# Kernel optimization log

Hardware: AMD Instinct MI355X
Metric: run time of the kernel (lower is better)

## Reference

```python
import jax, jax.numpy as jnp
import numpy as np

IOU_THRESHOLD = 0.5


def _make_boxes(key, n, canvas=800.0, min_size=8.0, max_size=160.0):
    k1, k2 = jax.random.split(key)
    cxy = jax.random.uniform(k1, (n, 2), dtype=jnp.float32) * canvas
    wh = min_size + jax.random.uniform(k2, (n, 2), dtype=jnp.float32) * (max_size - min_size)
    return jnp.concatenate([cxy - 0.5 * wh, cxy + 0.5 * wh], axis=1)  # [n,4] x1,y1,x2,y2


def setup_inputs() -> dict:
    key = jax.random.key(0)
    kp, kg, kl = jax.random.split(key, 3)
    N, M = 262144, 256
    proposals = _make_boxes(kp, N)
    gt_boxes = _make_boxes(kg, M)
    gt_labels = jax.random.randint(kl, (M,), 1, 21, dtype=jnp.int64)  # foreground classes 1..20
    return {"proposals": proposals, "gt_boxes": gt_boxes, "gt_labels": gt_labels}


def box_iou(a, b):
    # a: [N,4], b: [M,4] in x1,y1,x2,y2 -> [N,M]
    area_a = (a[:, 2] - a[:, 0]) * (a[:, 3] - a[:, 1])
    area_b = (b[:, 2] - b[:, 0]) * (b[:, 3] - b[:, 1])
    lt = jnp.maximum(a[:, None, :2], b[None, :, :2])
    rb = jnp.minimum(a[:, None, 2:], b[None, :, 2:])
    wh = jnp.clip(rb - lt, 0.0)
    inter = wh[..., 0] * wh[..., 1]
    union = area_a[:, None] + area_b[None, :] - inter
    return inter / union


def encode_boxes(props, gts):
    pw = props[:, 2] - props[:, 0]
    ph = props[:, 3] - props[:, 1]
    px = props[:, 0] + 0.5 * pw
    py = props[:, 1] + 0.5 * ph
    gw = gts[:, 2] - gts[:, 0]
    gh = gts[:, 3] - gts[:, 1]
    gx = gts[:, 0] + 0.5 * gw
    gy = gts[:, 1] + 0.5 * gh
    tx = (gx - px) / pw
    ty = (gy - py) / ph
    tw = jnp.log(gw / pw)
    th = jnp.log(gh / ph)
    return jnp.stack([tx, ty, tw, th], axis=1)


@jax.jit
def reference(proposals, gt_boxes, gt_labels):
    iou = box_iou(proposals, gt_boxes)            # [N,M] -- the memory-bound intermediate
    max_iou = jnp.max(iou, axis=1)                # [N]
    max_idx = jnp.argmax(iou, axis=1)             # [N]
    pos_mask = max_iou >= IOU_THRESHOLD
    roi_labels = jnp.where(pos_mask, gt_labels[max_idx], jnp.zeros_like(gt_labels[max_idx]))
    matched_gt = gt_boxes[max_idx]                # [N,4]
    deltas = encode_boxes(proposals, matched_gt)  # [N,4]
    roi_reg_targets = jnp.where(pos_mask[:, None], deltas, jnp.zeros_like(deltas))
    return roi_labels, roi_reg_targets
```

## Files before the change

### kernel.cpp

```cpp
#include <hip/hip_runtime.h>

#define M_GT 256

__global__ __launch_bounds__(256) void roi_assign_kernel(
    const float4* __restrict__ proposals,
    const float4* __restrict__ gt_boxes,
    const int*    __restrict__ gt_labels,
    float*        __restrict__ out_labels,
    float4*       __restrict__ out_deltas,
    int N)
{
    __shared__ float4 s_box[M_GT];
    __shared__ float  s_area[M_GT];

    int tid = threadIdx.x;
    float4 g0 = gt_boxes[tid];
    s_box[tid]  = g0;
    s_area[tid] = (g0.z - g0.x) * (g0.w - g0.y);
    __syncthreads();

    int p_local = tid >> 1;
    int part    = tid & 1;
    int i = blockIdx.x * 128 + p_local;
    if (i >= N) return;

    float4 p = proposals[i];
    float areaA = (p.z - p.x) * (p.w - p.y);

    int jbase = part << 7;
    float biE = -1.f, bSE = 1.f; int bxE = jbase;
    float biO = -1.f, bSO = 1.f; int bxO = jbase + 1;

    const float2* s_area2 = reinterpret_cast<const float2*>(s_area);

#pragma unroll 8
    for (int k = 0; k < 64; ++k) {
        int j = jbase + (k << 1);
        float4 gE = s_box[j];
        float4 gO = s_box[j + 1];
        float2 ar = s_area2[j >> 1];

        {
            float lx = fmaxf(p.x, gE.x), ly = fmaxf(p.y, gE.y);
            float rx = fminf(p.z, gE.z), ry = fminf(p.w, gE.w);
            float w = fmaxf(rx - lx, 0.f), h = fmaxf(ry - ly, 0.f);
            float inter = w * h;
            float S = areaA + ar.x;
            bool upd = (inter * bSE) > (biE * S);
            biE = upd ? inter : biE;
            bSE = upd ? S     : bSE;
            bxE = upd ? j     : bxE;
        }
        {
            float lx = fmaxf(p.x, gO.x), ly = fmaxf(p.y, gO.y);
            float rx = fminf(p.z, gO.z), ry = fminf(p.w, gO.w);
            float w = fmaxf(rx - lx, 0.f), h = fmaxf(ry - ly, 0.f);
            float inter = w * h;
            float S = areaA + ar.y;
            bool upd = (inter * bSO) > (biO * S);
            biO = upd ? inter : biO;
            bSO = upd ? S     : bSO;
            bxO = upd ? j + 1 : bxO;
        }
    }

    float ca = biO * bSE, cb = biE * bSO;
    bool takeO = (ca > cb) || ((ca == cb) && (bxO < bxE));
    float bi = takeO ? biO : biE;
    float bS = takeO ? bSO : bSE;
    int   bx = takeO ? bxO : bxE;

    float o_bi = __shfl_xor(bi, 1);
    float o_bS = __shfl_xor(bS, 1);
    int   o_bx = __shfl_xor(bx, 1);

    float b0i = part ? o_bi : bi,  b1i = part ? bi : o_bi;
    float b0S = part ? o_bS : bS,  b1S = part ? bS : o_bS;
    int   b0x = part ? o_bx : bx,  b1x = part ? bx : o_bx;

    bool take1 = (b1i * b0S) > (b0i * b1S);
    float mI = take1 ? b1i : b0i;
    float mS = take1 ? b1S : b0S;
    int   mx = take1 ? b1x : b0x;

    float uni = mS - mI;
    float iou = mI / uni;
    bool pos = (iou >= 0.5f);

    if (part == 0) {
        out_labels[i] = pos ? (float)gt_labels[mx] : 0.0f;
    } else {
        float4 g = s_box[mx];
        float pw = p.z - p.x, ph = p.w - p.y;
        float px = p.x + 0.5f * pw, py = p.y + 0.5f * ph;
        float gw = g.z - g.x, gh = g.w - g.y;
        float gx = g.x + 0.5f * gw, gy = g.y + 0.5f * gh;
        float4 d;
        if (pos) {
            d.x = (gx - px) / pw;
            d.y = (gy - py) / ph;
            d.z = logf(gw / pw);
            d.w = logf(gh / ph);
        } else {
            d.x = 0.f; d.y = 0.f; d.z = 0.f; d.w = 0.f;
        }
        out_deltas[i] = d;
    }
}

extern "C" void kernel_launch(void* const* d_in, const int* in_sizes, int n_in,
                              void* d_out, int out_size, void* d_ws, size_t ws_size,
                              hipStream_t stream) {
    const float4* proposals = (const float4*)d_in[0];
    const float4* gt_boxes  = (const float4*)d_in[1];
    const int*    gt_labels = (const int*)d_in[2];

    int N = in_sizes[0] / 4;

    float*  out_labels = (float*)d_out;
    float4* out_deltas = (float4*)((float*)d_out + N);

    dim3 block(256);
    dim3 grid((N + 127) / 128);
    roi_assign_kernel<<<grid, block, 0, stream>>>(
        proposals, gt_boxes, gt_labels, out_labels, out_deltas, N);
}
```

Baseline: 94.51 us.

## Assign one proposal per thread with four-way ILP and prefetched LDS reads

Each thread now scans all 256 ground-truth boxes for a single proposal instead of splitting the scan across two threads and merging with a shuffle. The loop keeps four independent running argmax accumulators, prefetches the next four boxes and areas from shared memory one step ahead, and then merges the accumulators at the end. This halves the grid, removes the cross-lane shuffle and the divergent output branch, and amortizes the shared-memory setup over twice as many proposals. In exchange each thread does twice the serial work and uses more registers. Fewer waves may also hide latency less well, and the occupancy hint of 4 blocks per SIMD-unit constrains register allocation.

```diff
diff --git a/kernel.cpp b/kernel.cpp
--- a/kernel.cpp
+++ b/kernel.cpp
@@ -2,7 +2,7 @@
 
 #define M_GT 256
 
-__global__ __launch_bounds__(256) void roi_assign_kernel(
+__global__ __launch_bounds__(256, 4) void roi_assign_kernel(
     const float4* __restrict__ proposals,
     const float4* __restrict__ gt_boxes,
     const int*    __restrict__ gt_labels,
@@ -19,93 +19,87 @@
     s_area[tid] = (g0.z - g0.x) * (g0.w - g0.y);
     __syncthreads();
 
-    int p_local = tid >> 1;
-    int part    = tid & 1;
-    int i = blockIdx.x * 128 + p_local;
+    int i = blockIdx.x * blockDim.x + tid;
     if (i >= N) return;
 
     float4 p = proposals[i];
     float areaA = (p.z - p.x) * (p.w - p.y);
 
-    int jbase = part << 7;
-    float biE = -1.f, bSE = 1.f; int bxE = jbase;
-    float biO = -1.f, bSO = 1.f; int bxO = jbase + 1;
+    float bi0 = -1.f, bS0 = 1.f; int bk0 = 0;
+    float bi1 = -1.f, bS1 = 1.f; int bk1 = 1;
+    float bi2 = -1.f, bS2 = 1.f; int bk2 = 2;
+    float bi3 = -1.f, bS3 = 1.f; int bk3 = 3;
 
-    const float2* s_area2 = reinterpret_cast<const float2*>(s_area);
+    const float4* s_area4 = reinterpret_cast<const float4*>(s_area);
 
-#pragma unroll 8
-    for (int k = 0; k < 64; ++k) {
-        int j = jbase + (k << 1);
-        float4 gE = s_box[j];
-        float4 gO = s_box[j + 1];
-        float2 ar = s_area2[j >> 1];
+#define STEP(g, av, BI, BS, BK, JJ)                                   \
+    { float lx = fmaxf(p.x, (g).x), ly = fmaxf(p.y, (g).y);           \
+      float rx = fminf(p.z, (g).z), ry = fminf(p.w, (g).w);           \
+      float w = fmaxf(rx - lx, 0.f), h = fmaxf(ry - ly, 0.f);         \
+      float inter = w * h;                                            \
+      float S = areaA + (av);                                         \
+      bool upd = (inter * BS) > (BI * S);                             \
+      BI = upd ? inter : BI;                                          \
+      BS = upd ? S     : BS;                                          \
+      BK = upd ? (JJ)  : BK; }
 
-        {
-            float lx = fmaxf(p.x, gE.x), ly = fmaxf(p.y, gE.y);
-            float rx = fminf(p.z, gE.z), ry = fminf(p.w, gE.w);
-            float w = fmaxf(rx - lx, 0.f), h = fmaxf(ry - ly, 0.f);
-            float inter = w * h;
-            float S = areaA + ar.x;
-            bool upd = (inter * bSE) > (biE * S);
-            biE = upd ? inter : biE;
-            bSE = upd ? S     : bSE;
-            bxE = upd ? j     : bxE;
-        }
-        {
-            float lx = fmaxf(p.x, gO.x), ly = fmaxf(p.y, gO.y);
-            float rx = fminf(p.z, gO.z), ry = fminf(p.w, gO.w);
-            float w = fmaxf(rx - lx, 0.f), h = fmaxf(ry - ly, 0.f);
-            float inter = w * h;
-            float S = areaA + ar.y;
-            bool upd = (inter * bSO) > (biO * S);
-            biO = upd ? inter : biO;
-            bSO = upd ? S     : bSO;
-            bxO = upd ? j + 1 : bxO;
-        }
+    float4 c0 = s_box[0], c1 = s_box[1], c2 = s_box[2], c3 = s_box[3];
+    float4 aq = s_area4[0];
+
+#pragma unroll 2
+    for (int m = 0; m < 64; ++m) {
+        int nb = (m + 1) & 63;
+        float4 n0 = s_box[nb * 4 + 0];
+        float4 n1 = s_box[nb * 4 + 1];
+        float4 n2 = s_box[nb * 4 + 2];
+        float4 n3 = s_box[nb * 4 + 3];
+        float4 na = s_area4[nb];
+
+        int j = m << 2;
+        STEP(c0, aq.x, bi0, bS0, bk0, j)
+        STEP(c1, aq.y, bi1, bS1, bk1, j + 1)
+        STEP(c2, aq.z, bi2, bS2, bk2, j + 2)
+        STEP(c3, aq.w, bi3, bS3, bk3, j + 3)
+
+        c0 = n0; c1 = n1; c2 = n2; c3 = n3; aq = na;
     }
+#undef STEP
 
-    float ca = biO * bSE, cb = biE * bSO;
-    bool takeO = (ca > cb) || ((ca == cb) && (bxO < bxE));
-    float bi = takeO ? biO : biE;
-    float bS = takeO ? bSO : bSE;
-    int   bx = takeO ? bxO : bxE;
+#define MERGE(Ai, AS, Ak, Bi, BS, Bk)                                 \
+    { float ca = (Bi) * (AS), cb = (Ai) * (BS);                       \
+      bool t = (ca > cb) || ((ca == cb) && ((Bk) < (Ak)));            \
+      Ai = t ? (Bi) : (Ai);                                           \
+      AS = t ? (BS) : (AS);                                           \
+      Ak = t ? (Bk) : (Ak); }
 
-    float o_bi = __shfl_xor(bi, 1);
-    float o_bS = __shfl_xor(bS, 1);
-    int   o_bx = __shfl_xor(bx, 1);
+    MERGE(bi0, bS0, bk0, bi1, bS1, bk1)
+    MERGE(bi2, bS2, bk2, bi3, bS3, bk3)
+    MERGE(bi0, bS0, bk0, bi2, bS2, bk2)
+#undef MERGE
 
-    float b0i = part ? o_bi : bi,  b1i = part ? bi : o_bi;
-    float b0S = part ? o_bS : bS,  b1S = part ? bS : o_bS;
-    int   b0x = part ? o_bx : bx,  b1x = part ? bx : o_bx;
+    float uni = bS0 - bi0;
+    float iou = bi0 / uni;
+    bool pos = (iou >= 0.5f);
+    int  mx  = bk0;
 
-    bool take1 = (b1i * b0S) > (b0i * b1S);
-    float mI = take1 ? b1i : b0i;
-    float mS = take1 ? b1S : b0S;
-    int   mx = take1 ? b1x : b0x;
+    out_labels[i] = pos ? (float)gt_labels[mx] : 0.0f;
 
-    float uni = mS - mI;
-    float iou = mI / uni;
-    bool pos = (iou >= 0.5f);
+    float4 g = s_box[mx];
+    float pw = p.z - p.x, ph = p.w - p.y;
+    float px = p.x + 0.5f * pw, py = p.y + 0.5f * ph;
+    float gw = g.z - g.x, gh = g.w - g.y;
+    float gx = g.x + 0.5f * gw, gy = g.y + 0.5f * gh;
 
-    if (part == 0) {
-        out_labels[i] = pos ? (float)gt_labels[mx] : 0.0f;
+    float4 d;
+    if (pos) {
+        d.x = (gx - px) / pw;
+        d.y = (gy - py) / ph;
+        d.z = logf(gw / pw);
+        d.w = logf(gh / ph);
     } else {
-        float4 g = s_box[mx];
-        float pw = p.z - p.x, ph = p.w - p.y;
-        float px = p.x + 0.5f * pw, py = p.y + 0.5f * ph;
-        float gw = g.z - g.x, gh = g.w - g.y;
-        float gx = g.x + 0.5f * gw, gy = g.y + 0.5f * gh;
-        float4 d;
-        if (pos) {
-            d.x = (gx - px) / pw;
-            d.y = (gy - py) / ph;
-            d.z = logf(gw / pw);
-            d.w = logf(gh / ph);
-        } else {
-            d.x = 0.f; d.y = 0.f; d.z = 0.f; d.w = 0.f;
-        }
-        out_deltas[i] = d;
+        d.x = 0.f; d.y = 0.f; d.z = 0.f; d.w = 0.f;
     }
+    out_deltas[i] = d;
 }
 
 extern "C" void kernel_launch(void* const* d_in, const int* in_sizes, int n_in,
@@ -121,7 +115,7 @@
     float4* out_deltas = (float4*)((float*)d_out + N);
 
     dim3 block(256);
-    dim3 grid((N + 127) / 128);
+    dim3 grid((N + 255) / 256);
     roi_assign_kernel<<<grid, block, 0, stream>>>(
         proposals, gt_boxes, gt_labels, out_labels, out_deltas, N);
 }
```

Result: no change. 93.18 us (-1.4%).
